# Performance work log

Hardware: AMD Instinct MI355X
Metric: run time of the kernel (lower is better)

## Reference

```python
import jax, jax.numpy as jnp
import numpy as np

K = 16  # neighborhood size


def _eigen_ratio(pts, k):
    """pts: [B, N, 3] -> ratio lambda_max / lambda_mid per point, [B, N]."""
    pts = pts[..., :3]
    # pairwise squared distances [B, N, N]
    sq = jnp.sum(pts * pts, axis=-1)  # [B, N]
    d2 = sq[:, :, None] + sq[:, None, :] - 2.0 * jnp.einsum('bnd,bmd->bnm', pts, pts)
    # k nearest neighbors (self included, as in KNN(x, x))
    _, idx = jax.lax.top_k(-d2, k)  # idx: [B, N, k] int32
    # gather neighbor coordinates: [B, N, k, 3]
    neighbors = jax.vmap(lambda p, i: p[i])(pts, idx)
    mean = jnp.mean(neighbors, axis=2, keepdims=True)
    diff = neighbors - mean  # [B, N, k, 3]
    # covariance = mean over k of outer products -> [B, N, 3, 3]
    cov = jnp.einsum('bnki,bnkj->bnij', diff, diff) / k
    ev = jnp.linalg.eigvalsh(cov)  # ascending: [..., 3]
    return ev[..., 2] / ev[..., 1]


def setup_inputs() -> dict:
    key = jax.random.key(0)
    kx, ky = jax.random.split(key)
    x = jax.random.normal(kx, (2, 8192, 3), dtype=jnp.float32)
    y = jax.random.normal(ky, (2, 8192, 3), dtype=jnp.float32)
    return {"x": x, "y": y}


def reference(x, y):
    er1 = _eigen_ratio(x, K)  # [B, N]
    er2 = _eigen_ratio(y, K)
    res = jnp.mean((er1 - er2) ** 2, axis=-1)  # mean over points
    return jnp.mean(res)  # reduction='mean' over batch
```

## Files before the change

### kernel.cpp

```cpp
#include <hip/hip_runtime.h>
#include <hip/hip_bf16.h>
#include <math.h>

#define NPTS   8192
#define KNN    16
#define G      16
#define NCELL  (G * G * G)
#define NCHUNK 128

__constant__ float c_B[17] = {
    -1e30f,
    -1.5341205f, -1.1503494f, -0.8871466f, -0.6744898f, -0.4887764f,
    -0.3186394f, -0.1573107f,  0.0f,        0.1573107f,  0.3186394f,
     0.4887764f,  0.6744898f,  0.8871466f,  1.1503494f,  1.5341205f,
     1e30f
};

__device__ __forceinline__ int cellOf(float v) {
    int c = 0;
#pragma unroll
    for (int i = 1; i <= 15; ++i) c += (v >= c_B[i]) ? 1 : 0;
    return c;
}

__device__ __forceinline__ int spread3(int v) {
    v = (v | (v << 4)) & 0x0C3;
    v = (v | (v << 2)) & 0x249;
    return v;
}

__device__ __forceinline__ int mortonCell(float px, float py, float pz) {
    return (spread3(cellOf(px)) << 2) | (spread3(cellOf(py)) << 1) | spread3(cellOf(pz));
}

__device__ __forceinline__ float dpp_prev_f(float v) {
    int r = __builtin_amdgcn_update_dpp(0, __float_as_int(v), 0x111, 0xF, 0xF, false);
    return __int_as_float(r);
}
__device__ __forceinline__ int dpp_prev_i(int v) {
    return __builtin_amdgcn_update_dpp(0, v, 0x111, 0xF, 0xF, false);
}

__device__ __forceinline__ float sum16(float v) {
    int b;
    b = __builtin_amdgcn_update_dpp(0, __float_as_int(v), 0xB1, 0xF, 0xF, false);
    v += __int_as_float(b);
    b = __builtin_amdgcn_update_dpp(0, __float_as_int(v), 0x4E, 0xF, 0xF, false);
    v += __int_as_float(b);
    b = __builtin_amdgcn_update_dpp(0, __float_as_int(v), 0x141, 0xF, 0xF, false);
    v += __int_as_float(b);
    b = __builtin_amdgcn_update_dpp(0, __float_as_int(v), 0x140, 0xF, 0xF, false);
    v += __int_as_float(b);
    return v;
}

__device__ __forceinline__ unsigned int waveMinU32(unsigned int v) {
    const int ID = (int)0xFFFFFFFF;
    int t;
    t = __builtin_amdgcn_update_dpp(ID, (int)v, 0xB1,  0xF, 0xF, false); v = min(v, (unsigned)t);
    t = __builtin_amdgcn_update_dpp(ID, (int)v, 0x4E,  0xF, 0xF, false); v = min(v, (unsigned)t);
    t = __builtin_amdgcn_update_dpp(ID, (int)v, 0x141, 0xF, 0xF, false); v = min(v, (unsigned)t);
    t = __builtin_amdgcn_update_dpp(ID, (int)v, 0x140, 0xF, 0xF, false); v = min(v, (unsigned)t);
    t = __builtin_amdgcn_update_dpp(ID, (int)v, 0x142, 0xF, 0xF, false); v = min(v, (unsigned)t);
    t = __builtin_amdgcn_update_dpp(ID, (int)v, 0x143, 0xF, 0xF, false); v = min(v, (unsigned)t);
    return (unsigned int)__builtin_amdgcn_readlane((int)v, 63);
}

__global__ __launch_bounds__(256) void countscan_kernel(
    const float* __restrict__ x, const float* __restrict__ y,
    unsigned int* __restrict__ cellpart, unsigned int* __restrict__ cellcnt,
    unsigned int* __restrict__ cnt4) {

    __shared__ unsigned int h[NCELL];
    __shared__ unsigned int scanbuf[256];
    __shared__ bool islast;

    const int tid   = threadIdx.x;
    const int cloud = blockIdx.x >> 2;
    const int part  = blockIdx.x & 3;
    const float* __restrict__ src = (cloud < 2 ? x : y) + (size_t)(cloud & 1) * NPTS * 3;

    for (int i = tid; i < NCELL; i += 256) h[i] = 0;
    __syncthreads();
#pragma unroll
    for (int k = 0; k < 8; ++k) {
        int p = (part << 11) | (k << 8) | tid;
        atomicAdd(&h[mortonCell(src[3 * p], src[3 * p + 1], src[3 * p + 2])], 1u);
    }
    __syncthreads();
    unsigned int* cp = cellpart + ((cloud << 2) | part) * NCELL;
    for (int i = tid; i < NCELL; i += 256) cp[i] = h[i];

    __threadfence();
    __syncthreads();
    if (tid == 0) {
        unsigned int t = atomicAdd(&cnt4[cloud], 1u);
        islast = ((t & 3u) == 3u);
    }
    __syncthreads();
    if (!islast) return;
    __threadfence();

    const unsigned int* base = cellpart + (cloud << 2) * NCELL;
    unsigned int cnt[16];
    unsigned int ssum = 0;
#pragma unroll
    for (int j = 0; j < 16; ++j) {
        int cell = (tid << 4) | j;
        unsigned int s = base[cell] + base[NCELL + cell]
                       + base[2 * NCELL + cell] + base[3 * NCELL + cell];
        cnt[j] = s; ssum += s;
    }
    scanbuf[tid] = ssum;
    __syncthreads();
    for (int d = 1; d < 256; d <<= 1) {
        unsigned int a = scanbuf[tid];
        unsigned int w = (tid >= d) ? scanbuf[tid - d] : 0;
        __syncthreads();
        scanbuf[tid] = a + w;
        __syncthreads();
    }
    unsigned int run = scanbuf[tid] - ssum;
    unsigned int* cc = cellcnt + cloud * NCELL;
#pragma unroll
    for (int j = 0; j < 16; ++j) {
        int cell = (tid << 4) | j;
        cc[cell] = run;
        run += cnt[j];
    }
}

__global__ __launch_bounds__(256) void scatter_kernel(
    const float* __restrict__ x, const float* __restrict__ y,
    unsigned int* __restrict__ cellcnt,
    float4* __restrict__ Ps, unsigned short* __restrict__ origids) {

    const int tid   = threadIdx.x;
    const int cloud = blockIdx.x >> 2;
    const int part  = blockIdx.x & 3;
    const float* __restrict__ src = (cloud < 2 ? x : y) + (size_t)(cloud & 1) * NPTS * 3;
    unsigned int* cc = cellcnt + cloud * NCELL;

#pragma unroll
    for (int k = 0; k < 8; ++k) {
        int p = (part << 11) | (k << 8) | tid;
        float px = src[3 * p], py = src[3 * p + 1], pz = src[3 * p + 2];
        int c = mortonCell(px, py, pz);
        unsigned int pos = atomicAdd(&cc[c], 1u);
        Ps[(cloud << 13) + pos] = make_float4(-2.f * px, -2.f * py, -2.f * pz,
                                              px * px + py * py + pz * pz);
        origids[(cloud << 13) + pos] = (unsigned short)p;
    }
}

__global__ __launch_bounds__(256) void aabb_kernel(
    const float4* __restrict__ Ps, float* __restrict__ aabbG ) {

    const int tid  = threadIdx.x;
    const int lane = tid & 63;
    const int w    = (blockIdx.x << 2) | (tid >> 6);
    const int cloud = w >> 7;
    const int c     = w & 127;

    float4 f = Ps[(cloud << 13) | (c << 6) | lane];
    float px = -0.5f * f.x, py = -0.5f * f.y, pz = -0.5f * f.z;
    float lx = px, hx = px, ly = py, hy = py, lz = pz, hz = pz;
#pragma unroll
    for (int s = 1; s < 64; s <<= 1) {
        lx = fminf(lx, __shfl_xor(lx, s)); hx = fmaxf(hx, __shfl_xor(hx, s));
        ly = fminf(ly, __shfl_xor(ly, s)); hy = fmaxf(hy, __shfl_xor(hy, s));
        lz = fminf(lz, __shfl_xor(lz, s)); hz = fmaxf(hz, __shfl_xor(hz, s));
    }
    if (lane == 0) {
        float* ab = aabbG + cloud * (6 * NCHUNK);
        ab[0 * NCHUNK + c] = lx; ab[1 * NCHUNK + c] = hx;
        ab[2 * NCHUNK + c] = ly; ab[3 * NCHUNK + c] = hy;
        ab[4 * NCHUNK + c] = lz; ab[5 * NCHUNK + c] = hz;
    }
}

__global__ __launch_bounds__(64) void knn_cov_kernel(
    const float4* __restrict__ Ps, const unsigned short* __restrict__ origids,
    const float* __restrict__ aabbG, float* __restrict__ cov,
    unsigned int* __restrict__ counter) {

    const int lane = threadIdx.x;
    const int wid  = blockIdx.x;
    const int cloud = wid >> 13;
    const int s     = wid & (NPTS - 1);

    if (wid == 0 && lane == 0) *counter = 0;

    const float4* __restrict__ Pc = Ps + (cloud << 13);
    const float* __restrict__ ab = aabbG + cloud * (6 * NCHUNK);
    const float4 qp = Pc[s];
    const float sqq = qp.w;
    const float qx = -0.5f * qp.x, qy = -0.5f * qp.y, qz = -0.5f * qp.z;
    const int co = s >> 6;

    float bval[2];
#pragma unroll
    for (int g = 0; g < 2; ++g) {
        int c = (g << 6) | lane;
        float dxl = fmaxf(0.f, fmaxf(ab[c] - qx, qx - ab[NCHUNK + c]));
        float dyl = fmaxf(0.f, fmaxf(ab[2 * NCHUNK + c] - qy, qy - ab[3 * NCHUNK + c]));
        float dzl = fmaxf(0.f, fmaxf(ab[4 * NCHUNK + c] - qz, qz - ab[5 * NCHUNK + c]));
        bval[g] = dxl * dxl + dyl * dyl + dzl * dzl;
    }
    unsigned long long rem0 = ~0ull, rem1 = ~0ull;
    if (co < 64) rem0 &= ~(1ull << co); else rem1 &= ~(1ull << (co - 64));

    auto keys_of = [&](unsigned long long l0, unsigned long long l1,
                       unsigned int& k0, unsigned int& k1) {
        k0 = ((l0 >> lane) & 1)
            ? ((__float_as_uint(bval[0]) & 0xFFFFFF80u) | (unsigned)lane) : 0xFFFFFFFFu;
        k1 = ((l1 >> lane) & 1)
            ? ((__float_as_uint(bval[1]) & 0xFFFFFF80u) | (unsigned)(64 + lane)) : 0xFFFFFFFFu;
    };
    auto argmin2 = [&](unsigned long long l0, unsigned long long l1,
                       int& cidA, int& cidB, bool& hasB) {
        unsigned int k0, k1;
        keys_of(l0, l1, k0, k1);
        unsigned int a = waveMinU32(min(k0, k1));
        cidA = (int)(a & 127u);
        if (lane == (cidA & 63)) { if (cidA < 64) k0 = 0xFFFFFFFFu; else k1 = 0xFFFFFFFFu; }
        unsigned int b = waveMinU32(min(k0, k1));
        hasB = (b != 0xFFFFFFFFu); cidB = (int)(b & 127u);
    };
    auto clear_rem = [&](int cid) {
        if (cid < 64) rem0 &= ~(1ull << cid); else rem1 &= ~(1ull << (cid - 64));
    };
    auto bound_of = [&](int cid) {
        return __int_as_float(__builtin_amdgcn_readlane(
            __float_as_int(bval[cid >> 6]), cid & 63));
    };
    auto popPair = [&](unsigned long long& l0, unsigned long long& l1,
                       int& cA, int& cB, bool& hB) {
        if (__popcll(l0) + __popcll(l1) <= 2) {
            if (l0) { cA = __builtin_ctzll(l0); l0 &= l0 - 1; }
            else    { cA = 64 + __builtin_ctzll(l1); l1 &= l1 - 1; }
            if (l0)      { cB = __builtin_ctzll(l0); l0 &= l0 - 1; hB = true; }
            else if (l1) { cB = 64 + __builtin_ctzll(l1); l1 &= l1 - 1; hB = true; }
            else hB = false;
        } else {
            argmin2(l0, l1, cA, cB, hB);
            if (cA < 64) l0 &= ~(1ull << cA); else l1 &= ~(1ull << (cA - 64));
            if (hB) { if (cB < 64) l0 &= ~(1ull << cB); else l1 &= ~(1ull << (cB - 64)); }
        }
        clear_rem(cA);
        if (hB) clear_rem(cB);
    };

    unsigned long long t0 = rem0, t1 = rem1;
    int pA, pB; bool hPB;
    popPair(t0, t1, pA, pB, hPB);
    float4 pfA = Pc[(pA << 6) | lane];
    float4 pfB = Pc[(pB << 6) | lane];

    float valV, thr;
    int   idxV;
    {
        int pos = (co << 6) | lane;
        float4 f = Pc[pos];
        float k = fmaf(qx, f.x, fmaf(qy, f.y, fmaf(qz, f.z, sqq + f.w)));
        int p = pos;
#pragma unroll
        for (int size = 2; size <= 64; size <<= 1) {
#pragma unroll
            for (int stride = size >> 1; stride >= 1; stride >>= 1) {
                float ok = __shfl_xor(k, stride);
                int   op = __shfl_xor(p, stride);
                bool up = ((lane & size) == 0);
                bool lower = ((lane & stride) == 0);
                bool want_min = (up == lower);
                bool take = want_min ? (ok < k) : (ok > k);
                k = take ? ok : k;
                p = take ? op : p;
            }
        }
        valV = __shfl(k, lane & 15);
        idxV = __shfl(p, lane & 15);
        thr  = __shfl(k, 15);
    }

    auto process = [&](float4 f, int cid) {
        float d2 = fmaf(qx, f.x, fmaf(qy, f.y, fmaf(qz, f.z, sqq + f.w)));
        unsigned long long m = __ballot(d2 < thr);
        while (m) {
            int li = __builtin_ctzll(m); m &= m - 1;
            float sv = __int_as_float(
                __builtin_amdgcn_readlane(__float_as_int(d2), li));
            if (sv < thr) {
                int sj = (cid << 6) | li;
                float pv = dpp_prev_f(valV);
                int   pi = dpp_prev_i(idxV);
                bool keep  = (valV <= sv);
                bool fromv = ((lane & 15) == 0) || (pv <= sv);
                float nv = keep ? valV : (fromv ? sv : pv);
                int   ni = keep ? idxV : (fromv ? sj : pi);
                valV = nv; idxV = ni;
                thr = __int_as_float(__builtin_amdgcn_readlane(__float_as_int(valV), 15));
            }
        }
    };

    if (bound_of(pA) < thr) process(pfA, pA);
    if (hPB && bound_of(pB) < thr) process(pfB, pB);

    for (;;) {
        unsigned long long live0 = rem0 & __ballot(bval[0] < thr);
        unsigned long long live1 = rem1 & __ballot(bval[1] < thr);
        if (!(live0 | live1)) break;

        int cidA, cidB; bool hasB;
        popPair(live0, live1, cidA, cidB, hasB);

        float4 fA = Pc[(cidA << 6) | lane];
        float4 fB;
        if (hasB) fB = Pc[(cidB << 6) | lane];

        process(fA, cidA);
        if (hasB && bound_of(cidB) < thr) process(fB, cidB);
    }

    float4 nf = Pc[idxV];
    float nx = -0.5f * nf.x, ny = -0.5f * nf.y, nz = -0.5f * nf.z;

    const float invk = 1.0f / KNN;
    float mx = sum16(nx) * invk;
    float my = sum16(ny) * invk;
    float mz = sum16(nz) * invk;

    float dx = nx - mx, dy = ny - my, dz = nz - mz;
    float c00 = sum16(dx * dx) * invk, c01 = sum16(dx * dy) * invk, c02 = sum16(dx * dz) * invk;
    float c11 = sum16(dy * dy) * invk, c12 = sum16(dy * dz) * invk, c22 = sum16(dz * dz) * invk;

    if (lane == 0) {
        int orig = origids[(cloud << 13) + s];
        float* cp = cov + ((size_t)(cloud << 13) + orig) * 6;
        *(float2*)(cp)     = make_float2(c00, c01);
        *(float2*)(cp + 2) = make_float2(c02, c11);
        *(float2*)(cp + 4) = make_float2(c12, c22);
    }
}

__device__ double eig_ratio(const float* __restrict__ cp) {
    double a00 = cp[0], a01 = cp[1], a02 = cp[2];
    double a11 = cp[3], a12 = cp[4], a22 = cp[5];

    double qm = (a00 + a11 + a22) * (1.0 / 3.0);
    double p1 = a01 * a01 + a02 * a02 + a12 * a12;
    double b00 = a00 - qm, b11 = a11 - qm, b22 = a22 - qm;
    double p2 = b00 * b00 + b11 * b11 + b22 * b22 + 2.0 * p1;

    if (p2 <= 0.0) return 1.0;
    double p = sqrt(p2 * (1.0 / 6.0));
    double inv = 1.0 / p;
    double m00 = b00 * inv, m11 = b11 * inv, m22 = b22 * inv;
    double m01 = a01 * inv, m02 = a02 * inv, m12 = a12 * inv;
    double detB = m00 * (m11 * m22 - m12 * m12)
                - m01 * (m01 * m22 - m12 * m02)
                + m02 * (m01 * m12 - m11 * m02);
    double r = 0.5 * detB;
    r = fmin(1.0, fmax(-1.0, r));
    double phi = acos(r) * (1.0 / 3.0);
    double e1 = qm + 2.0 * p * cos(phi);
    double e3 = qm + 2.0 * p * cos(phi + 2.0943951023931953);
    double e2 = 3.0 * qm - e1 - e3;
    return e1 / e2;
}

#define EIG_BLOCKS 64

__global__ __launch_bounds__(256) void eigred_kernel(const float* __restrict__ cov,
                                                     double* __restrict__ partial,
                                                     unsigned int* __restrict__ counter,
                                                     float* __restrict__ out) {
    __shared__ double sb[256];
    __shared__ bool islast;
    const int i = blockIdx.x * 256 + threadIdx.x;
    double r1 = eig_ratio(cov + (size_t)i * 6);
    double r2 = eig_ratio(cov + (size_t)(2 * NPTS + i) * 6);
    double d = r1 - r2;
    sb[threadIdx.x] = d * d;
    __syncthreads();
    for (int s2 = 128; s2 > 0; s2 >>= 1) {
        if (threadIdx.x < s2) sb[threadIdx.x] += sb[threadIdx.x + s2];
        __syncthreads();
    }
    if (threadIdx.x == 0) {
        partial[blockIdx.x] = sb[0];
        __threadfence();
        islast = (atomicAdd(counter, 1u) == EIG_BLOCKS - 1);
    }
    __syncthreads();
    if (islast && threadIdx.x < 64) {
        __threadfence();
        double v = ((volatile double*)partial)[threadIdx.x];
#pragma unroll
        for (int w = 1; w < 64; w <<= 1) v += __shfl_xor(v, w);
        if (threadIdx.x == 0) out[0] = (float)(v / (double)(2 * NPTS));
    }
}

extern "C" void kernel_launch(void* const* d_in, const int* in_sizes, int n_in,
                              void* d_out, int out_size, void* d_ws, size_t ws_size,
                              hipStream_t stream) {
    const float* x = (const float*)d_in[0];
    const float* y = (const float*)d_in[1];
    char* ws = (char*)d_ws;

    float4*         Ps       = (float4*)(ws);
    unsigned short* origids  = (unsigned short*)(ws + 524288);
    float*          aabbG    = (float*)(ws + 589824);
    float*          cov      = (float*)(ws + 602112);
    unsigned int*   cellcnt  = (unsigned int*)(ws + 1388544);
    unsigned int*   cellpart = (unsigned int*)(ws + 1454080);
    double*         partial  = (double*)(ws + 1716224);
    unsigned int*   counter  = (unsigned int*)(ws + 1716736);
    unsigned int*   cnt4     = (unsigned int*)(ws + 1716740);
    float*          out      = (float*)d_out;

    countscan_kernel<<<16, 256, 0, stream>>>(x, y, cellpart, cellcnt, cnt4);
    scatter_kernel<<<16, 256, 0, stream>>>(x, y, cellcnt, Ps, origids);
    aabb_kernel<<<128, 256, 0, stream>>>(Ps, aabbG);
    knn_cov_kernel<<<4 * NPTS, 64, 0, stream>>>(Ps, origids, aabbG, cov, counter);
    eigred_kernel<<<EIG_BLOCKS, 256, 0, stream>>>(cov, partial, counter, out);
}
```

Baseline: 91.00 us.

## Interleave two KNN queries per wavefront to overlap their memory latency

Each 64-lane block now handles two query points, one from the first half of the clouds and one from the second, with the grid halved to match. The two queries' chunk loads and candidate processing are interleaved in a shared loop so one query's gathers can overlap the other's latency. The cost is higher register pressure from duplicated state. Warp divergence also grows, since the loop runs until both queries finish.

```diff
diff --git a/kernel.cpp b/kernel.cpp
--- a/kernel.cpp
+++ b/kernel.cpp
@@ -185,56 +185,71 @@
     unsigned int* __restrict__ counter) {
 
     const int lane = threadIdx.x;
-    const int wid  = blockIdx.x;
-    const int cloud = wid >> 13;
-    const int s     = wid & (NPTS - 1);
-
-    if (wid == 0 && lane == 0) *counter = 0;
-
-    const float4* __restrict__ Pc = Ps + (cloud << 13);
-    const float* __restrict__ ab = aabbG + cloud * (6 * NCHUNK);
-    const float4 qp = Pc[s];
-    const float sqq = qp.w;
-    const float qx = -0.5f * qp.x, qy = -0.5f * qp.y, qz = -0.5f * qp.z;
-    const int co = s >> 6;
-
-    float bval[2];
-#pragma unroll
-    for (int g = 0; g < 2; ++g) {
-        int c = (g << 6) | lane;
-        float dxl = fmaxf(0.f, fmaxf(ab[c] - qx, qx - ab[NCHUNK + c]));
-        float dyl = fmaxf(0.f, fmaxf(ab[2 * NCHUNK + c] - qy, qy - ab[3 * NCHUNK + c]));
-        float dzl = fmaxf(0.f, fmaxf(ab[4 * NCHUNK + c] - qz, qz - ab[5 * NCHUNK + c]));
-        bval[g] = dxl * dxl + dyl * dyl + dzl * dzl;
-    }
-    unsigned long long rem0 = ~0ull, rem1 = ~0ull;
-    if (co < 64) rem0 &= ~(1ull << co); else rem1 &= ~(1ull << (co - 64));
-
-    auto keys_of = [&](unsigned long long l0, unsigned long long l1,
-                       unsigned int& k0, unsigned int& k1) {
-        k0 = ((l0 >> lane) & 1)
-            ? ((__float_as_uint(bval[0]) & 0xFFFFFF80u) | (unsigned)lane) : 0xFFFFFFFFu;
-        k1 = ((l1 >> lane) & 1)
-            ? ((__float_as_uint(bval[1]) & 0xFFFFFF80u) | (unsigned)(64 + lane)) : 0xFFFFFFFFu;
-    };
-    auto argmin2 = [&](unsigned long long l0, unsigned long long l1,
+    const int widA = blockIdx.x;
+    const int widB = blockIdx.x + 2 * NPTS;
+
+    if (widA == 0 && lane == 0) *counter = 0;
+
+    struct QS {
+        const float4* Pc;
+        const float*  ab;
+        float qx, qy, qz, sqq;
+        float b0, b1;
+        unsigned long long rem0, rem1;
+        float valV, thr;
+        int idxV, co;
+    };
+    QS A, B;
+
+    auto setup = [&](QS& q, int wid_) {
+        int cloud = wid_ >> 13, s = wid_ & (NPTS - 1);
+        q.Pc = Ps + (cloud << 13);
+        q.ab = aabbG + cloud * (6 * NCHUNK);
+        float4 qp = q.Pc[s];
+        q.sqq = qp.w;
+        q.qx = -0.5f * qp.x; q.qy = -0.5f * qp.y; q.qz = -0.5f * qp.z;
+        q.co = s >> 6;
+    };
+
+    auto init_bounds = [&](QS& q) {
+        {
+            int c = lane;
+            float dxl = fmaxf(0.f, fmaxf(q.ab[c] - q.qx, q.qx - q.ab[NCHUNK + c]));
+            float dyl = fmaxf(0.f, fmaxf(q.ab[2 * NCHUNK + c] - q.qy, q.qy - q.ab[3 * NCHUNK + c]));
+            float dzl = fmaxf(0.f, fmaxf(q.ab[4 * NCHUNK + c] - q.qz, q.qz - q.ab[5 * NCHUNK + c]));
+            q.b0 = dxl * dxl + dyl * dyl + dzl * dzl;
+        }
+        {
+            int c = 64 | lane;
+            float dxl = fmaxf(0.f, fmaxf(q.ab[c] - q.qx, q.qx - q.ab[NCHUNK + c]));
+            float dyl = fmaxf(0.f, fmaxf(q.ab[2 * NCHUNK + c] - q.qy, q.qy - q.ab[3 * NCHUNK + c]));
+            float dzl = fmaxf(0.f, fmaxf(q.ab[4 * NCHUNK + c] - q.qz, q.qz - q.ab[5 * NCHUNK + c]));
+            q.b1 = dxl * dxl + dyl * dyl + dzl * dzl;
+        }
+        q.rem0 = ~0ull; q.rem1 = ~0ull;
+        if (q.co < 64) q.rem0 &= ~(1ull << q.co); else q.rem1 &= ~(1ull << (q.co - 64));
+    };
+
+    auto argmin2 = [&](QS& q, unsigned long long l0, unsigned long long l1,
                        int& cidA, int& cidB, bool& hasB) {
-        unsigned int k0, k1;
-        keys_of(l0, l1, k0, k1);
+        unsigned int k0 = ((l0 >> lane) & 1)
+            ? ((__float_as_uint(q.b0) & 0xFFFFFF80u) | (unsigned)lane) : 0xFFFFFFFFu;
+        unsigned int k1 = ((l1 >> lane) & 1)
+            ? ((__float_as_uint(q.b1) & 0xFFFFFF80u) | (unsigned)(64 + lane)) : 0xFFFFFFFFu;
         unsigned int a = waveMinU32(min(k0, k1));
         cidA = (int)(a & 127u);
         if (lane == (cidA & 63)) { if (cidA < 64) k0 = 0xFFFFFFFFu; else k1 = 0xFFFFFFFFu; }
         unsigned int b = waveMinU32(min(k0, k1));
         hasB = (b != 0xFFFFFFFFu); cidB = (int)(b & 127u);
     };
-    auto clear_rem = [&](int cid) {
-        if (cid < 64) rem0 &= ~(1ull << cid); else rem1 &= ~(1ull << (cid - 64));
-    };
-    auto bound_of = [&](int cid) {
-        return __int_as_float(__builtin_amdgcn_readlane(
-            __float_as_int(bval[cid >> 6]), cid & 63));
-    };
-    auto popPair = [&](unsigned long long& l0, unsigned long long& l1,
+    auto clear_rem = [&](QS& q, int cid) {
+        if (cid < 64) q.rem0 &= ~(1ull << cid); else q.rem1 &= ~(1ull << (cid - 64));
+    };
+    auto bound_of = [&](QS& q, int cid) {
+        float bsel = (cid < 64) ? q.b0 : q.b1;
+        return __int_as_float(__builtin_amdgcn_readlane(__float_as_int(bsel), cid & 63));
+    };
+    auto popPair = [&](QS& q, unsigned long long& l0, unsigned long long& l1,
                        int& cA, int& cB, bool& hB) {
         if (__popcll(l0) + __popcll(l1) <= 2) {
             if (l0) { cA = __builtin_ctzll(l0); l0 &= l0 - 1; }
@@ -243,27 +258,17 @@
             else if (l1) { cB = 64 + __builtin_ctzll(l1); l1 &= l1 - 1; hB = true; }
             else hB = false;
         } else {
-            argmin2(l0, l1, cA, cB, hB);
+            argmin2(q, l0, l1, cA, cB, hB);
             if (cA < 64) l0 &= ~(1ull << cA); else l1 &= ~(1ull << (cA - 64));
             if (hB) { if (cB < 64) l0 &= ~(1ull << cB); else l1 &= ~(1ull << (cB - 64)); }
         }
-        clear_rem(cA);
-        if (hB) clear_rem(cB);
-    };
-
-    unsigned long long t0 = rem0, t1 = rem1;
-    int pA, pB; bool hPB;
-    popPair(t0, t1, pA, pB, hPB);
-    float4 pfA = Pc[(pA << 6) | lane];
-    float4 pfB = Pc[(pB << 6) | lane];
-
-    float valV, thr;
-    int   idxV;
-    {
-        int pos = (co << 6) | lane;
-        float4 f = Pc[pos];
-        float k = fmaf(qx, f.x, fmaf(qy, f.y, fmaf(qz, f.z, sqq + f.w)));
-        int p = pos;
+        clear_rem(q, cA);
+        if (hB) clear_rem(q, cB);
+    };
+
+    auto seed = [&](QS& q, float4 f) {
+        float k = fmaf(q.qx, f.x, fmaf(q.qy, f.y, fmaf(q.qz, f.z, q.sqq + f.w)));
+        int p = (q.co << 6) | lane;
 #pragma unroll
         for (int size = 2; size <= 64; size <<= 1) {
 #pragma unroll
@@ -278,70 +283,103 @@
                 p = take ? op : p;
             }
         }
-        valV = __shfl(k, lane & 15);
-        idxV = __shfl(p, lane & 15);
-        thr  = __shfl(k, 15);
-    }
-
-    auto process = [&](float4 f, int cid) {
-        float d2 = fmaf(qx, f.x, fmaf(qy, f.y, fmaf(qz, f.z, sqq + f.w)));
-        unsigned long long m = __ballot(d2 < thr);
+        q.valV = __shfl(k, lane & 15);
+        q.idxV = __shfl(p, lane & 15);
+        q.thr  = __shfl(k, 15);
+    };
+
+    auto process = [&](QS& q, float4 f, int cid) {
+        float d2 = fmaf(q.qx, f.x, fmaf(q.qy, f.y, fmaf(q.qz, f.z, q.sqq + f.w)));
+        unsigned long long m = __ballot(d2 < q.thr);
         while (m) {
             int li = __builtin_ctzll(m); m &= m - 1;
             float sv = __int_as_float(
                 __builtin_amdgcn_readlane(__float_as_int(d2), li));
-            if (sv < thr) {
+            if (sv < q.thr) {
                 int sj = (cid << 6) | li;
-                float pv = dpp_prev_f(valV);
-                int   pi = dpp_prev_i(idxV);
-                bool keep  = (valV <= sv);
+                float pv = dpp_prev_f(q.valV);
+                int   pi = dpp_prev_i(q.idxV);
+                bool keep  = (q.valV <= sv);
                 bool fromv = ((lane & 15) == 0) || (pv <= sv);
-                float nv = keep ? valV : (fromv ? sv : pv);
-                int   ni = keep ? idxV : (fromv ? sj : pi);
-                valV = nv; idxV = ni;
-                thr = __int_as_float(__builtin_amdgcn_readlane(__float_as_int(valV), 15));
+                float nv = keep ? q.valV : (fromv ? sv : pv);
+                int   ni = keep ? q.idxV : (fromv ? sj : pi);
+                q.valV = nv; q.idxV = ni;
+                q.thr = __int_as_float(__builtin_amdgcn_readlane(__float_as_int(q.valV), 15));
             }
         }
     };
 
-    if (bound_of(pA) < thr) process(pfA, pA);
-    if (hPB && bound_of(pB) < thr) process(pfB, pB);
+    setup(A, widA); setup(B, widB);
+    init_bounds(A); init_bounds(B);
+
+    int pA1, pA2, pB1, pB2; bool hA2, hB2;
+    { unsigned long long t0 = A.rem0, t1 = A.rem1; popPair(A, t0, t1, pA1, pA2, hA2); }
+    { unsigned long long t0 = B.rem0, t1 = B.rem1; popPair(B, t0, t1, pB1, pB2, hB2); }
+    float4 pfA1 = A.Pc[(pA1 << 6) | lane];
+    float4 pfA2 = A.Pc[(pA2 << 6) | lane];
+    float4 pfB1 = B.Pc[(pB1 << 6) | lane];
+    float4 pfB2 = B.Pc[(pB2 << 6) | lane];
+    float4 ownA = A.Pc[(A.co << 6) | lane];
+    float4 ownB = B.Pc[(B.co << 6) | lane];
+
+    seed(A, ownA);
+    seed(B, ownB);
+
+    if (bound_of(A, pA1) < A.thr) process(A, pfA1, pA1);
+    if (hA2 && bound_of(A, pA2) < A.thr) process(A, pfA2, pA2);
+    if (bound_of(B, pB1) < B.thr) process(B, pfB1, pB1);
+    if (hB2 && bound_of(B, pB2) < B.thr) process(B, pfB2, pB2);
 
     for (;;) {
-        unsigned long long live0 = rem0 & __ballot(bval[0] < thr);
-        unsigned long long live1 = rem1 & __ballot(bval[1] < thr);
-        if (!(live0 | live1)) break;
-
-        int cidA, cidB; bool hasB;
-        popPair(live0, live1, cidA, cidB, hasB);
-
-        float4 fA = Pc[(cidA << 6) | lane];
-        float4 fB;
-        if (hasB) fB = Pc[(cidB << 6) | lane];
-
-        process(fA, cidA);
-        if (hasB && bound_of(cidB) < thr) process(fB, cidB);
-    }
-
-    float4 nf = Pc[idxV];
-    float nx = -0.5f * nf.x, ny = -0.5f * nf.y, nz = -0.5f * nf.z;
-
-    const float invk = 1.0f / KNN;
-    float mx = sum16(nx) * invk;
-    float my = sum16(ny) * invk;
-    float mz = sum16(nz) * invk;
-
-    float dx = nx - mx, dy = ny - my, dz = nz - mz;
-    float c00 = sum16(dx * dx) * invk, c01 = sum16(dx * dy) * invk, c02 = sum16(dx * dz) * invk;
-    float c11 = sum16(dy * dy) * invk, c12 = sum16(dy * dz) * invk, c22 = sum16(dz * dz) * invk;
-
-    if (lane == 0) {
-        int orig = origids[(cloud << 13) + s];
-        float* cp = cov + ((size_t)(cloud << 13) + orig) * 6;
-        *(float2*)(cp)     = make_float2(c00, c01);
-        *(float2*)(cp + 2) = make_float2(c02, c11);
-        *(float2*)(cp + 4) = make_float2(c12, c22);
-    }
+        unsigned long long a0 = A.rem0 & __ballot(A.b0 < A.thr);
+        unsigned long long a1 = A.rem1 & __ballot(A.b1 < A.thr);
+        unsigned long long b0 = B.rem0 & __ballot(B.b0 < B.thr);
+        unsigned long long b1 = B.rem1 & __ballot(B.b1 < B.thr);
+        bool hA = (a0 | a1) != 0, hB = (b0 | b1) != 0;
+        if (!hA && !hB) break;
+
+        int cA1 = 0, cA2 = 0, cB1 = 0, cB2 = 0;
+        bool hA2r = false, hB2r = false;
+        if (hA) popPair(A, a0, a1, cA1, cA2, hA2r);
+        if (hB) popPair(B, b0, b1, cB1, cB2, hB2r);
+
+        float4 fA1, fA2, fB1, fB2;
+        if (hA) { fA1 = A.Pc[(cA1 << 6) | lane]; if (hA2r) fA2 = A.Pc[(cA2 << 6) | lane]; }
+        if (hB) { fB1 = B.Pc[(cB1 << 6) | lane]; if (hB2r) fB2 = B.Pc[(cB2 << 6) | lane]; }
+
+        if (hA) {
+            process(A, fA1, cA1);
+            if (hA2r && bound_of(A, cA2) < A.thr) process(A, fA2, cA2);
+        }
+        if (hB) {
+            process(B, fB1, cB1);
+            if (hB2r && bound_of(B, cB2) < B.thr) process(B, fB2, cB2);
+        }
+    }
+
+    float4 nfA = A.Pc[A.idxV];
+    float4 nfB = B.Pc[B.idxV];
+
+    auto finish = [&](QS& q, float4 nf, int wid_) {
+        float nx = -0.5f * nf.x, ny = -0.5f * nf.y, nz = -0.5f * nf.z;
+        const float invk = 1.0f / KNN;
+        float mx = sum16(nx) * invk;
+        float my = sum16(ny) * invk;
+        float mz = sum16(nz) * invk;
+        float dx = nx - mx, dy = ny - my, dz = nz - mz;
+        float c00 = sum16(dx * dx) * invk, c01 = sum16(dx * dy) * invk, c02 = sum16(dx * dz) * invk;
+        float c11 = sum16(dy * dy) * invk, c12 = sum16(dy * dz) * invk, c22 = sum16(dz * dz) * invk;
+        if (lane == 0) {
+            int cloud = wid_ >> 13, s = wid_ & (NPTS - 1);
+            int orig = origids[(cloud << 13) + s];
+            float* cp = cov + ((size_t)(cloud << 13) + orig) * 6;
+            *(float2*)(cp)     = make_float2(c00, c01);
+            *(float2*)(cp + 2) = make_float2(c02, c11);
+            *(float2*)(cp + 4) = make_float2(c12, c22);
+        }
+    };
+    finish(A, nfA, widA);
+    finish(B, nfB, widB);
 }
 
 __device__ double eig_ratio(const float* __restrict__ cp) {
@@ -424,6 +462,6 @@
     countscan_kernel<<<16, 256, 0, stream>>>(x, y, cellpart, cellcnt, cnt4);
     scatter_kernel<<<16, 256, 0, stream>>>(x, y, cellcnt, Ps, origids);
     aabb_kernel<<<128, 256, 0, stream>>>(Ps, aabbG);
-    knn_cov_kernel<<<4 * NPTS, 64, 0, stream>>>(Ps, origids, aabbG, cov, counter);
+    knn_cov_kernel<<<2 * NPTS, 64, 0, stream>>>(Ps, origids, aabbG, cov, counter);
     eigred_kernel<<<EIG_BLOCKS, 256, 0, stream>>>(cov, partial, counter, out);
 }
```

Measured after the change: 96.27 us. 5.8% more time.
